# Performance work log

Measured on AMD Instinct MI355X. Metric: run time of the kernel, lower is better.

## Reference

```python
import jax, jax.numpy as jnp
import numpy as np

N, D, H, N_HEADS = 2048, 512, 512, 16

def setup_inputs() -> dict:
    key = jax.random.key(0)
    k1, k2, k3 = jax.random.split(key, 3)
    inputs = jax.random.normal(k1, (N, D), dtype=jnp.float32)
    idx = jax.random.randint(k2, (N,), 0, N_HEADS, dtype=jnp.int64)
    weights = jax.random.normal(k3, (N_HEADS, D, H), dtype=jnp.float32)
    biases = jnp.zeros((N_HEADS, H), dtype=jnp.float32)
    return {"inputs": inputs, "idx": idx, "weights": weights, "biases": biases}

def reference(inputs, idx, weights, biases):
    # per-sample weight gather: (N, D, H) then batched vec-mat: (N, 1, D) @ (N, D, H) -> (N, H)
    w = weights[idx]            # (N, D, H)  -- the redundant materialized gather
    b = biases[idx]             # (N, H)
    return jnp.einsum('nd,ndh->nh', inputs, w) + b
```

## Files before the change

### kernel.cpp

```cpp
#include <hip/hip_runtime.h>


#define N_SAMPLES 2048
#define DIM       512
#define HDIM      512
#define N_HEADS   16
#define SH        32
#define BPITCH    520

typedef __attribute__((ext_vector_type(8))) short bf16x8;
typedef __attribute__((ext_vector_type(4))) float floatx4;

__device__ inline unsigned short f2bf_rne(float f) {
    union { float f; unsigned u; } v; v.f = f;
    return (unsigned short)((v.u + 0x7FFFu + ((v.u >> 16) & 1u)) >> 16);
}
__device__ inline unsigned bfpack_rne(float lo, float hi) {
    return (unsigned)f2bf_rne(lo) | ((unsigned)f2bf_rne(hi) << 16);
}

__global__ __launch_bounds__(256) void xconv(const float* __restrict__ x,
                                             unsigned* __restrict__ xb) {
    const int i = blockIdx.x * 256 + threadIdx.x;
    const float4 v0 = *(const float4*)(x + i * 8);
    const float4 v1 = *(const float4*)(x + i * 8 + 4);
    uint4 o;
    o.x = bfpack_rne(v0.x, v0.y);
    o.y = bfpack_rne(v0.z, v0.w);
    o.z = bfpack_rne(v1.x, v1.y);
    o.w = bfpack_rne(v1.z, v1.w);
    *(uint4*)(xb + i * 4) = o;
}

__global__ __launch_bounds__(256, 2) void fused(
    const unsigned short* __restrict__ xb,
    const int*   __restrict__ idx,
    const float* __restrict__ w,
    const float* __restrict__ bias,
    float*       __restrict__ out)
{
    __shared__ unsigned short Bl[SH * BPITCH];
    __shared__ unsigned short slist[N_SAMPLES];
    __shared__ int wcnt[4];

    const int bid  = blockIdx.x;
    const int head = bid >> 4;
    const int h0   = (bid & 15) * SH;
    const int t    = threadIdx.x;
    const int wave = t >> 6;
    const int lane = t & 63;
    const int l16  = lane & 15;
    const int quad = lane >> 4;

    int myidx[8];
    #pragma unroll
    for (int c = 0; c < 8; ++c)
        myidx[c] = idx[(wave * 8 + c) * 64 + lane];

    const int hh = (t & 7) * 4;
    const int dg = t >> 3;
    const float* wg = w + (size_t)head * DIM * HDIM + h0;
    float4 q[16];
    #pragma unroll
    for (int s = 0; s < 16; ++s)
        q[s] = *(const float4*)(wg + (size_t)(dg * 16 + s) * HDIM + hh);

    unsigned long long masks[8];
    {
        int mycnt = 0;
        #pragma unroll
        for (int c = 0; c < 8; ++c) {
            masks[c] = __ballot(myidx[c] == head);
            mycnt += __popcll(masks[c]);
        }
        if (lane == 0) wcnt[wave] = mycnt;
    }
    __syncthreads();
    int cnt = 0, base = 0;
    #pragma unroll
    for (int i = 0; i < 4; ++i) { if (i < wave) base += wcnt[i]; cnt += wcnt[i]; }
    {
        int pos = base;
        #pragma unroll
        for (int c = 0; c < 8; ++c) {
            const unsigned long long m = masks[c];
            if (m & (1ull << lane)) {
                const int rank = __popcll(m & ((1ull << lane) - 1ull));
                slist[pos + rank] = (unsigned short)((wave * 8 + c) * 64 + lane);
            }
            pos += __popcll(m);
        }
    }

    #pragma unroll
    for (int p = 0; p < 8; ++p) {
        const int d = dg * 16 + 2 * p;
        const float4 qa = q[2 * p], qb = q[2 * p + 1];
        *(unsigned*)&Bl[(hh + 0) * BPITCH + d] = bfpack_rne(qa.x, qb.x);
        *(unsigned*)&Bl[(hh + 1) * BPITCH + d] = bfpack_rne(qa.y, qb.y);
        *(unsigned*)&Bl[(hh + 2) * BPITCH + d] = bfpack_rne(qa.z, qb.z);
        *(unsigned*)&Bl[(hh + 3) * BPITCH + d] = bfpack_rne(qa.w, qb.w);
    }
    __syncthreads();

    const int   mt  = (cnt + 15) >> 4;
    const float bv0 = bias[head * HDIM + h0 + l16];
    const float bv1 = bias[head * HDIM + h0 + 16 + l16];

    int j = wave;
    bf16x8 a[16];
    if (j < mt) {
        const int mg  = j * 16 + l16;
        const int row = slist[mg < cnt ? mg : cnt - 1];
        const unsigned short* ap = xb + (size_t)row * DIM + quad * 8;
        #pragma unroll
        for (int ks = 0; ks < 16; ++ks) a[ks] = *(const bf16x8*)(ap + ks * 32);
    }
    for (; j < mt; j += 4) {
        bf16x8 an[16];
        const int jn = j + 4;
        if (jn < mt) {
            const int mg  = jn * 16 + l16;
            const int row = slist[mg < cnt ? mg : cnt - 1];
            const unsigned short* ap = xb + (size_t)row * DIM + quad * 8;
            #pragma unroll
            for (int ks = 0; ks < 16; ++ks) an[ks] = *(const bf16x8*)(ap + ks * 32);
        }

        floatx4 acc0 = {0.f, 0.f, 0.f, 0.f};
        floatx4 acc1 = {0.f, 0.f, 0.f, 0.f};
        #pragma unroll
        for (int ks = 0; ks < 16; ++ks) {
            const bf16x8 b0 = *(const bf16x8*)&Bl[l16 * BPITCH + ks * 32 + quad * 8];
            const bf16x8 b1 = *(const bf16x8*)&Bl[(16 + l16) * BPITCH + ks * 32 + quad * 8];
            acc0 = __builtin_amdgcn_mfma_f32_16x16x32_bf16(a[ks], b0, acc0, 0, 0, 0);
            acc1 = __builtin_amdgcn_mfma_f32_16x16x32_bf16(a[ks], b1, acc1, 0, 0, 0);
        }

        #pragma unroll
        for (int r = 0; r < 4; ++r) {
            const int mm = j * 16 + quad * 4 + r;
            if (mm < cnt) {
                const int rg = slist[mm];
                out[(size_t)rg * HDIM + h0 + l16]      = acc0[r] + bv0;
                out[(size_t)rg * HDIM + h0 + 16 + l16] = acc1[r] + bv1;
            }
        }

        #pragma unroll
        for (int ks = 0; ks < 16; ++ks) a[ks] = an[ks];
    }
}

extern "C" void kernel_launch(void* const* d_in, const int* in_sizes, int n_in,
                              void* d_out, int out_size, void* d_ws, size_t ws_size,
                              hipStream_t stream) {
    const float* x   = (const float*)d_in[0];
    const int*   idx = (const int*)  d_in[1];
    const float* w   = (const float*)d_in[2];
    const float* b   = (const float*)d_in[3];
    float*       out = (float*)d_out;

    unsigned* xb = (unsigned*)d_ws;

    xconv<<<512, 256, 0, stream>>>(x, xb);
    fused<<<N_HEADS * (HDIM / SH), 256, 0, stream>>>((const unsigned short*)xb, idx, w, b, out);
}
```

Baseline: 87.64 us.

## Fuse input bf16 conversion into main kernel and drop separate conversion pass

Removes the standalone kernel that converted inputs to bf16 in workspace. The fused kernel now loads fp32 input rows directly and packs them to bf16 in registers using truncation via byte-permute instead of round-to-nearest-even. The software prefetch of the next tile's A operand is also dropped. This saves a launch and a full-array round trip, but doubles the bytes read per A load, removes load/compute overlap, and slightly changes numerics through truncation.

```diff
diff --git a/kernel.cpp b/kernel.cpp
--- a/kernel.cpp
+++ b/kernel.cpp
@@ -18,22 +18,20 @@
 __device__ inline unsigned bfpack_rne(float lo, float hi) {
     return (unsigned)f2bf_rne(lo) | ((unsigned)f2bf_rne(hi) << 16);
 }
-
-__global__ __launch_bounds__(256) void xconv(const float* __restrict__ x,
-                                             unsigned* __restrict__ xb) {
-    const int i = blockIdx.x * 256 + threadIdx.x;
-    const float4 v0 = *(const float4*)(x + i * 8);
-    const float4 v1 = *(const float4*)(x + i * 8 + 4);
-    uint4 o;
-    o.x = bfpack_rne(v0.x, v0.y);
-    o.y = bfpack_rne(v0.z, v0.w);
-    o.z = bfpack_rne(v1.x, v1.y);
-    o.w = bfpack_rne(v1.z, v1.w);
-    *(uint4*)(xb + i * 4) = o;
+__device__ inline unsigned bf2_trunc(float lo, float hi) {
+    return __builtin_amdgcn_perm(__float_as_uint(hi), __float_as_uint(lo), 0x07060302u);
+}
+__device__ inline bf16x8 pack_a(const float4 u0, const float4 u1) {
+    union { bf16x8 v; unsigned u[4]; } r;
+    r.u[0] = bf2_trunc(u0.x, u0.y);
+    r.u[1] = bf2_trunc(u0.z, u0.w);
+    r.u[2] = bf2_trunc(u1.x, u1.y);
+    r.u[3] = bf2_trunc(u1.z, u1.w);
+    return r.v;
 }
 
 __global__ __launch_bounds__(256, 2) void fused(
-    const unsigned short* __restrict__ xb,
+    const float* __restrict__ x,
     const int*   __restrict__ idx,
     const float* __restrict__ w,
     const float* __restrict__ bias,
@@ -107,24 +105,30 @@
     const float bv0 = bias[head * HDIM + h0 + l16];
     const float bv1 = bias[head * HDIM + h0 + 16 + l16];
 
-    int j = wave;
-    bf16x8 a[16];
-    if (j < mt) {
+    for (int j = wave; j < mt; j += 4) {
         const int mg  = j * 16 + l16;
         const int row = slist[mg < cnt ? mg : cnt - 1];
-        const unsigned short* ap = xb + (size_t)row * DIM + quad * 8;
-        #pragma unroll
-        for (int ks = 0; ks < 16; ++ks) a[ks] = *(const bf16x8*)(ap + ks * 32);
-    }
-    for (; j < mt; j += 4) {
-        bf16x8 an[16];
-        const int jn = j + 4;
-        if (jn < mt) {
-            const int mg  = jn * 16 + l16;
-            const int row = slist[mg < cnt ? mg : cnt - 1];
-            const unsigned short* ap = xb + (size_t)row * DIM + quad * 8;
+        const float* xp = x + (size_t)row * DIM + quad * 8;
+
+        bf16x8 a[16];
+        {
+            float4 u[16];
             #pragma unroll
-            for (int ks = 0; ks < 16; ++ks) an[ks] = *(const bf16x8*)(ap + ks * 32);
+            for (int ks = 0; ks < 8; ++ks) {
+                u[2 * ks]     = *(const float4*)(xp + ks * 32);
+                u[2 * ks + 1] = *(const float4*)(xp + ks * 32 + 4);
+            }
+            #pragma unroll
+            for (int ks = 0; ks < 8; ++ks)
+                a[ks] = pack_a(u[2 * ks], u[2 * ks + 1]);
+            #pragma unroll
+            for (int ks = 8; ks < 16; ++ks) {
+                u[2 * (ks - 8)]     = *(const float4*)(xp + ks * 32);
+                u[2 * (ks - 8) + 1] = *(const float4*)(xp + ks * 32 + 4);
+            }
+            #pragma unroll
+            for (int ks = 8; ks < 16; ++ks)
+                a[ks] = pack_a(u[2 * (ks - 8)], u[2 * (ks - 8) + 1]);
         }
 
         floatx4 acc0 = {0.f, 0.f, 0.f, 0.f};
@@ -146,9 +150,6 @@
                 out[(size_t)rg * HDIM + h0 + 16 + l16] = acc1[r] + bv1;
             }
         }
-
-        #pragma unroll
-        for (int ks = 0; ks < 16; ++ks) a[ks] = an[ks];
     }
 }
 
@@ -161,8 +162,5 @@
     const float* b   = (const float*)d_in[3];
     float*       out = (float*)d_out;
 
-    unsigned* xb = (unsigned*)d_ws;
-
-    xconv<<<512, 256, 0, stream>>>(x, xb);
-    fused<<<N_HEADS * (HDIM / SH), 256, 0, stream>>>((const unsigned short*)xb, idx, w, b, out);
+    fused<<<N_HEADS * (HDIM / SH), 256, 0, stream>>>(x, idx, w, b, out);
 }
```

Result: no change. 88.92 us (+1.5%).
